# Kernel optimization log

Hardware: AMD Instinct MI355X
Metric: run time of the kernel (lower is better)

The kernel has to match this reference:

```python
import jax, jax.numpy as jnp
import numpy as np

T, H, E, K, I = 4096, 1024, 8, 2, 2048
EPS = 1e-5


def setup_inputs() -> dict:
    key = jax.random.key(0)
    ks = jax.random.split(key, 5)
    xavier = jax.nn.initializers.variance_scaling(1.0, 'fan_avg', 'uniform', dtype=jnp.float32)
    return {
        'x': jax.random.normal(ks[0], (T, H), dtype=jnp.float32),
        'scale': jnp.ones((H,), dtype=jnp.float32),
        'gate_kernel': xavier(ks[1], (H, E), jnp.float32),
        'gate_bias': jnp.zeros((E,), dtype=jnp.float32),
        'mlp1_weight': xavier(ks[2], (E, 2 * I, H), jnp.float32),
        'mlp1_bias': jnp.zeros((E, 2 * I), dtype=jnp.float32),
        'mlp2_weight': xavier(ks[3], (E, H, I), jnp.float32),
        'mlp2_bias': jnp.zeros((E, H), dtype=jnp.float32),
    }


def reference(x, scale, gate_kernel, gate_bias, mlp1_weight, mlp1_bias, mlp2_weight, mlp2_bias):
    # RMSNorm in fp32
    t = x.astype(jnp.float32)
    rms = jnp.sqrt(jnp.mean(t * t, axis=-1, keepdims=True) + EPS)
    normed = ((t / rms) * scale).astype(x.dtype)  # [T, H]

    # Gating: top-k experts + softmax over selected logits
    gate_logits = normed @ gate_kernel + gate_bias  # [T, E]
    expert_logits, expert_indices = jax.lax.top_k(gate_logits, K)  # [T, K]
    expert_weights = jax.nn.softmax(expert_logits, axis=-1)  # [T, K]

    # Dense all-expert SwiGLU MLP (faithful to vmap-over-experts original)
    # mlp1_weight: [E, 2I, H] -> mlp1: [E, T, 2I]
    mlp1 = jnp.einsum('td,efd->etf', normed, mlp1_weight) + mlp1_bias[:, None, :]
    gate_part = jnp.minimum(mlp1[..., :I], 7.0)
    linear_part = jnp.clip(mlp1[..., I:], -7.0, 7.0)
    swish_gate = gate_part * jax.nn.sigmoid(1.702 * gate_part)
    activated = swish_gate * (linear_part + 1.0)  # [E, T, I]
    # mlp2_weight: [E, H, I] -> expert_outputs: [T, E, H]
    expert_outputs = (jnp.einsum('eti,ehi->eth', activated, mlp2_weight)
                      + mlp2_bias[:, None, :]).transpose(1, 0, 2)

    # Scatter top-k weights to dense [T, E] and combine
    one_hot = jax.nn.one_hot(expert_indices, E, dtype=expert_outputs.dtype)  # [T, K, E]
    dense_gate_weights = jnp.sum(one_hot * expert_weights[..., None], axis=1)  # [T, E]
    fused = jnp.einsum('teh,te->th', expert_outputs, dense_gate_weights)
    return x + fused
```

## Files before the change

kernel.cpp:

```cpp
#include <hip/hip_runtime.h>
#include <hip/hip_bf16.h>
#include <math.h>

#define T_ 4096
#define H_ 1024
#define E_ 8
#define I_ 2048
#define EPS_ 1e-5f
#define LDST 72

using bf16x8 = __attribute__((ext_vector_type(8))) short;
using f32x4  = __attribute__((ext_vector_type(4))) float;

static __device__ __forceinline__ unsigned short f2bf(float f) {
    union { float f; unsigned int u; } v; v.f = f;
    unsigned int u = v.u;
    u += 0x7fffu + ((u >> 16) & 1u);
    return (unsigned short)(u >> 16);
}

__global__ __launch_bounds__(256) void k_convert(
    const float* __restrict__ src, unsigned short* __restrict__ dst)
{
    size_t i = (size_t)blockIdx.x * 256 + threadIdx.x;
    const float4* s = (const float4*)src + i * 2;
    float4 a = s[0], b = s[1];
    ushort4 lo, hi;
    lo.x = f2bf(a.x); lo.y = f2bf(a.y); lo.z = f2bf(a.z); lo.w = f2bf(a.w);
    hi.x = f2bf(b.x); hi.y = f2bf(b.y); hi.z = f2bf(b.z); hi.w = f2bf(b.w);
    ((ushort4*)dst)[i * 2]     = lo;
    ((ushort4*)dst)[i * 2 + 1] = hi;
}

__global__ __launch_bounds__(256) void k_norm_gate(
    const float* __restrict__ x, const float* __restrict__ scale,
    const float* __restrict__ gk, const float* __restrict__ gb,
    unsigned short* __restrict__ normed_bf,
    int* __restrict__ counts, int* __restrict__ tok_list, float* __restrict__ w_list)
{
    int t = blockIdx.x;
    int tid = threadIdx.x;
    int lane = tid & 63, wave = tid >> 6;

    float4 xv = ((const float4*)(x + (size_t)t * H_))[tid];
    float ss = xv.x*xv.x + xv.y*xv.y + xv.z*xv.z + xv.w*xv.w;
    #pragma unroll
    for (int off = 32; off; off >>= 1) ss += __shfl_down(ss, off);

    __shared__ float red[4];
    __shared__ float s_inv;
    if (lane == 0) red[wave] = ss;
    __syncthreads();
    if (tid == 0) {
        float tot = red[0] + red[1] + red[2] + red[3];
        s_inv = 1.0f / sqrtf(tot / (float)H_ + EPS_);
    }
    __syncthreads();
    float inv = s_inv;

    float4 sv = ((const float4*)scale)[tid];
    float nv[4];
    nv[0] = xv.x*inv*sv.x; nv[1] = xv.y*inv*sv.y;
    nv[2] = xv.z*inv*sv.z; nv[3] = xv.w*inv*sv.w;
    ushort4 nb;
    nb.x = f2bf(nv[0]); nb.y = f2bf(nv[1]); nb.z = f2bf(nv[2]); nb.w = f2bf(nv[3]);
    ((ushort4*)(normed_bf + (size_t)t * H_))[tid] = nb;

    float p[E_];
    #pragma unroll
    for (int e = 0; e < E_; e++) p[e] = 0.f;
    int h0 = tid * 4;
    #pragma unroll
    for (int j = 0; j < 4; j++) {
        const float4* g4 = (const float4*)(gk + (size_t)(h0 + j) * E_);
        float4 a = g4[0], b = g4[1];
        float n = nv[j];
        p[0] += n*a.x; p[1] += n*a.y; p[2] += n*a.z; p[3] += n*a.w;
        p[4] += n*b.x; p[5] += n*b.y; p[6] += n*b.z; p[7] += n*b.w;
    }
    __shared__ float pr[E_][4];
    #pragma unroll
    for (int e = 0; e < E_; e++) {
        float v = p[e];
        #pragma unroll
        for (int off = 32; off; off >>= 1) v += __shfl_down(v, off);
        if (lane == 0) pr[e][wave] = v;
    }
    __syncthreads();
    if (tid == 0) {
        float lg[E_];
        #pragma unroll
        for (int e = 0; e < E_; e++)
            lg[e] = pr[e][0] + pr[e][1] + pr[e][2] + pr[e][3] + gb[e];
        int b0 = -1, b1 = -1; float l0 = -1e30f, l1 = -1e30f;
        #pragma unroll
        for (int e = 0; e < E_; e++) {
            if (lg[e] > l0) { l1 = l0; b1 = b0; l0 = lg[e]; b0 = e; }
            else if (lg[e] > l1) { l1 = lg[e]; b1 = e; }
        }
        float e1 = expf(l1 - l0);
        float w0 = 1.f / (1.f + e1);
        float w1 = e1 / (1.f + e1);
        int p0 = atomicAdd(&counts[b0], 1);
        tok_list[b0 * T_ + p0] = t * 2 + 0; w_list[b0 * T_ + p0] = w0;
        int p1 = atomicAdd(&counts[b1], 1);
        tok_list[b1 * T_ + p1] = t * 2 + 1; w_list[b1 * T_ + p1] = w1;
    }
}

__global__ __launch_bounds__(256) void k_init_out(
    const float* __restrict__ x, float* __restrict__ out)
{
    size_t i = (size_t)blockIdx.x * 256 + threadIdx.x;
    ((float4*)out)[i] = ((const float4*)x)[i];
}

template<bool PRE>
__global__ __launch_bounds__(256) void k_mlp1(
    const float* __restrict__ w1f, const unsigned short* __restrict__ w1b,
    const float* __restrict__ b1,
    const unsigned short* __restrict__ normed_bf,
    const int* __restrict__ counts, const int* __restrict__ tok_list,
    unsigned short* __restrict__ act)
{
    int e = blockIdx.z;
    int Ne = counts[e];
    int mt0 = blockIdx.y * 64;
    if (mt0 >= Ne) return;
    int it0 = blockIdx.x * 64;
    int tid = threadIdx.x;
    int lane = tid & 63, w = tid >> 6;
    int quad = lane >> 4, m16 = lane & 15;
    int wr = w >> 1, wc = w & 1;

    __shared__ unsigned short lA[64 * LDST];
    __shared__ unsigned short lBg[64 * LDST];
    __shared__ unsigned short lBl[64 * LDST];
    __shared__ int ls_tk[64];

    if (tid < 64) {
        int slot = mt0 + tid;
        ls_tk[tid] = (slot < Ne) ? tok_list[e * T_ + slot] : -1;
    }
    __syncthreads();

    f32x4 accg[2][2], accl[2][2];
    #pragma unroll
    for (int mi = 0; mi < 2; mi++)
        #pragma unroll
        for (int ni = 0; ni < 2; ni++) {
            accg[mi][ni] = (f32x4){0.f, 0.f, 0.f, 0.f};
            accl[mi][ni] = (f32x4){0.f, 0.f, 0.f, 0.f};
        }

    const size_t w1base = (size_t)e * 2 * I_ * H_;
    int rA = tid >> 3, sgA = tid & 7;
    int nB = tid >> 2, sgB = tid & 3;

    for (int kk = 0; kk < H_; kk += 64) {
        #pragma unroll
        for (int rr = 0; rr < 64; rr += 32) {
            int r = rA + rr;
            int tk = ls_tk[r];
            uint4 v = make_uint4(0u, 0u, 0u, 0u);
            if (tk >= 0)
                v = *(const uint4*)(normed_bf + (size_t)(tk >> 1) * H_ + kk + sgA * 8);
            *(uint4*)(&lA[r * LDST + sgA * 8]) = v;
        }
        if (PRE) {
            const unsigned short* srcg = w1b + w1base + (size_t)(it0 + nB) * H_ + kk + sgB * 16;
            const unsigned short* srcl = srcg + (size_t)I_ * H_;
            *(uint4*)(&lBg[nB * LDST + sgB * 16])     = ((const uint4*)srcg)[0];
            *(uint4*)(&lBg[nB * LDST + sgB * 16 + 8]) = ((const uint4*)srcg)[1];
            *(uint4*)(&lBl[nB * LDST + sgB * 16])     = ((const uint4*)srcl)[0];
            *(uint4*)(&lBl[nB * LDST + sgB * 16 + 8]) = ((const uint4*)srcl)[1];
        } else {
            const float* srcg = w1f + w1base + (size_t)(it0 + nB) * H_ + kk + sgB * 16;
            const float* srcl = srcg + (size_t)I_ * H_;
            unsigned short tg[16], tl[16];
            #pragma unroll
            for (int q = 0; q < 4; q++) {
                float4 fg = ((const float4*)srcg)[q];
                float4 fl = ((const float4*)srcl)[q];
                tg[q*4+0] = f2bf(fg.x); tg[q*4+1] = f2bf(fg.y);
                tg[q*4+2] = f2bf(fg.z); tg[q*4+3] = f2bf(fg.w);
                tl[q*4+0] = f2bf(fl.x); tl[q*4+1] = f2bf(fl.y);
                tl[q*4+2] = f2bf(fl.z); tl[q*4+3] = f2bf(fl.w);
            }
            *(uint4*)(&lBg[nB * LDST + sgB * 16])     = *(uint4*)(&tg[0]);
            *(uint4*)(&lBg[nB * LDST + sgB * 16 + 8]) = *(uint4*)(&tg[8]);
            *(uint4*)(&lBl[nB * LDST + sgB * 16])     = *(uint4*)(&tl[0]);
            *(uint4*)(&lBl[nB * LDST + sgB * 16 + 8]) = *(uint4*)(&tl[8]);
        }
        __syncthreads();
        #pragma unroll
        for (int ks = 0; ks < 64; ks += 32) {
            bf16x8 af[2], bg[2], bl[2];
            #pragma unroll
            for (int mi = 0; mi < 2; mi++)
                af[mi] = *(const bf16x8*)(&lA[(wr * 32 + mi * 16 + m16) * LDST + ks + quad * 8]);
            #pragma unroll
            for (int ni = 0; ni < 2; ni++) {
                bg[ni] = *(const bf16x8*)(&lBg[(wc * 32 + ni * 16 + m16) * LDST + ks + quad * 8]);
                bl[ni] = *(const bf16x8*)(&lBl[(wc * 32 + ni * 16 + m16) * LDST + ks + quad * 8]);
            }
            #pragma unroll
            for (int mi = 0; mi < 2; mi++)
                #pragma unroll
                for (int ni = 0; ni < 2; ni++) {
                    accg[mi][ni] = __builtin_amdgcn_mfma_f32_16x16x32_bf16(
                        af[mi], bg[ni], accg[mi][ni], 0, 0, 0);
                    accl[mi][ni] = __builtin_amdgcn_mfma_f32_16x16x32_bf16(
                        af[mi], bl[ni], accl[mi][ni], 0, 0, 0);
                }
        }
        __syncthreads();
    }

    const float* b1g = b1 + (size_t)e * 2 * I_;
    const float* b1l = b1g + I_;
    #pragma unroll
    for (int mi = 0; mi < 2; mi++) {
        #pragma unroll
        for (int reg = 0; reg < 4; reg++) {
            int row = wr * 32 + mi * 16 + quad * 4 + reg;
            int tk = ls_tk[row];
            if (tk < 0) continue;
            #pragma unroll
            for (int ni = 0; ni < 2; ni++) {
                int i = it0 + wc * 32 + ni * 16 + m16;
                float g = accg[mi][ni][reg] + b1g[i];
                float l = accl[mi][ni][reg] + b1l[i];
                g = fminf(g, 7.f);
                l = fminf(fmaxf(l, -7.f), 7.f);
                float sw = g / (1.f + expf(-1.702f * g));
                act[(size_t)tk * I_ + i] = f2bf(sw * (l + 1.f));
            }
        }
    }
}

template<bool PRE>
__global__ __launch_bounds__(256) void k_mlp2(
    const float* __restrict__ w2f, const unsigned short* __restrict__ w2b,
    const float* __restrict__ b2,
    const unsigned short* __restrict__ act,
    const int* __restrict__ counts, const int* __restrict__ tok_list,
    const float* __restrict__ w_list,
    float* __restrict__ out)
{
    int e = blockIdx.z;
    int Ne = counts[e];
    int mt0 = blockIdx.y * 64;
    if (mt0 >= Ne) return;
    int ht0 = blockIdx.x * 128;
    int tid = threadIdx.x;
    int lane = tid & 63, w = tid >> 6;
    int quad = lane >> 4, m16 = lane & 15;
    int wr = w >> 1, wc = w & 1;

    __shared__ unsigned short lA[64 * LDST];
    __shared__ unsigned short lB[128 * LDST];
    __shared__ int ls_tk[64];
    __shared__ float ls_w[64];

    if (tid < 64) {
        int slot = mt0 + tid;
        ls_tk[tid] = (slot < Ne) ? tok_list[e * T_ + slot] : -1;
        ls_w[tid]  = (slot < Ne) ? w_list[e * T_ + slot] : 0.f;
    }
    __syncthreads();

    f32x4 acc[2][4];
    #pragma unroll
    for (int mi = 0; mi < 2; mi++)
        #pragma unroll
        for (int ni = 0; ni < 4; ni++)
            acc[mi][ni] = (f32x4){0.f, 0.f, 0.f, 0.f};

    const size_t w2base = (size_t)e * H_ * I_;
    int rA = tid >> 3, sgA = tid & 7;
    int nB = tid >> 2, sgB = tid & 3;

    for (int kk = 0; kk < I_; kk += 64) {
        #pragma unroll
        for (int rr = 0; rr < 64; rr += 32) {
            int r = rA + rr;
            int tk = ls_tk[r];
            uint4 v = make_uint4(0u, 0u, 0u, 0u);
            if (tk >= 0)
                v = *(const uint4*)(act + (size_t)tk * I_ + kk + sgA * 8);
            *(uint4*)(&lA[r * LDST + sgA * 8]) = v;
        }
        #pragma unroll
        for (int rr = 0; rr < 128; rr += 64) {
            int r = nB + rr;
            if (PRE) {
                const unsigned short* src = w2b + w2base + (size_t)(ht0 + r) * I_ + kk + sgB * 16;
                *(uint4*)(&lB[r * LDST + sgB * 16])     = ((const uint4*)src)[0];
                *(uint4*)(&lB[r * LDST + sgB * 16 + 8]) = ((const uint4*)src)[1];
            } else {
                const float* src = w2f + w2base + (size_t)(ht0 + r) * I_ + kk + sgB * 16;
                unsigned short tb[16];
                #pragma unroll
                for (int q = 0; q < 4; q++) {
                    float4 f4 = ((const float4*)src)[q];
                    tb[q*4+0] = f2bf(f4.x); tb[q*4+1] = f2bf(f4.y);
                    tb[q*4+2] = f2bf(f4.z); tb[q*4+3] = f2bf(f4.w);
                }
                *(uint4*)(&lB[r * LDST + sgB * 16])     = *(uint4*)(&tb[0]);
                *(uint4*)(&lB[r * LDST + sgB * 16 + 8]) = *(uint4*)(&tb[8]);
            }
        }
        __syncthreads();
        #pragma unroll
        for (int ks = 0; ks < 64; ks += 32) {
            bf16x8 af[2], bf[4];
            #pragma unroll
            for (int mi = 0; mi < 2; mi++)
                af[mi] = *(const bf16x8*)(&lA[(wr * 32 + mi * 16 + m16) * LDST + ks + quad * 8]);
            #pragma unroll
            for (int ni = 0; ni < 4; ni++)
                bf[ni] = *(const bf16x8*)(&lB[(wc * 64 + ni * 16 + m16) * LDST + ks + quad * 8]);
            #pragma unroll
            for (int mi = 0; mi < 2; mi++)
                #pragma unroll
                for (int ni = 0; ni < 4; ni++)
                    acc[mi][ni] = __builtin_amdgcn_mfma_f32_16x16x32_bf16(
                        af[mi], bf[ni], acc[mi][ni], 0, 0, 0);
        }
        __syncthreads();
    }

    const float* b2e = b2 + (size_t)e * H_;
    #pragma unroll
    for (int mi = 0; mi < 2; mi++) {
        #pragma unroll
        for (int reg = 0; reg < 4; reg++) {
            int row = wr * 32 + mi * 16 + quad * 4 + reg;
            int tk = ls_tk[row];
            if (tk < 0) continue;
            int t = tk >> 1;
            float wgt = ls_w[row];
            #pragma unroll
            for (int ni = 0; ni < 4; ni++) {
                int h = ht0 + wc * 64 + ni * 16 + m16;
                float v = acc[mi][ni][reg] + b2e[h];
                atomicAdd(&out[(size_t)t * H_ + h], wgt * v);
            }
        }
    }
}

extern "C" void kernel_launch(void* const* d_in, const int* in_sizes, int n_in,
                              void* d_out, int out_size, void* d_ws, size_t ws_size,
                              hipStream_t stream) {
    const float* x     = (const float*)d_in[0];
    const float* scale = (const float*)d_in[1];
    const float* gk    = (const float*)d_in[2];
    const float* gb    = (const float*)d_in[3];
    const float* w1    = (const float*)d_in[4];
    const float* b1    = (const float*)d_in[5];
    const float* w2    = (const float*)d_in[6];
    const float* b2    = (const float*)d_in[7];
    float* out = (float*)d_out;

    char* ws = (char*)d_ws;
    const size_t MB = 1024 * 1024;
    bool pre = ws_size >= (size_t)138 * MB;

    unsigned short* normed_bf = (unsigned short*)ws;
    unsigned short* act       = (unsigned short*)(ws + 8 * MB);
    unsigned short* w1b = nullptr;
    unsigned short* w2b = nullptr;
    char* ctl;
    if (pre) {
        w1b = (unsigned short*)(ws + 40 * MB);
        w2b = (unsigned short*)(ws + 104 * MB);
        ctl = ws + 136 * MB;
    } else {
        ctl = ws + 40 * MB;
    }
    int*   counts   = (int*)ctl;
    int*   tok_list = (int*)(ctl + 256);
    float* w_list   = (float*)(ctl + 256 + (size_t)E_ * T_ * 4);

    hipMemsetAsync(counts, 0, E_ * sizeof(int), stream);

    k_norm_gate<<<dim3(T_), dim3(256), 0, stream>>>(x, scale, gk, gb,
                                                    normed_bf, counts, tok_list, w_list);
    if (pre) {
        k_convert<<<dim3((E_ * 2 * I_ * H_) / (256 * 8)), dim3(256), 0, stream>>>(w1, w1b);
        k_convert<<<dim3((E_ * H_ * I_) / (256 * 8)), dim3(256), 0, stream>>>(w2, w2b);
    }
    k_init_out<<<dim3(T_ * H_ / (256 * 4)), dim3(256), 0, stream>>>(x, out);

    if (pre) {
        k_mlp1<true><<<dim3(I_ / 64, T_ / 64, E_), dim3(256), 0, stream>>>(
            nullptr, w1b, b1, normed_bf, counts, tok_list, act);
        k_mlp2<true><<<dim3(H_ / 128, T_ / 64, E_), dim3(256), 0, stream>>>(
            nullptr, w2b, b2, act, counts, tok_list, w_list, out);
    } else {
        k_mlp1<false><<<dim3(I_ / 64, T_ / 64, E_), dim3(256), 0, stream>>>(
            w1, nullptr, b1, normed_bf, counts, tok_list, act);
        k_mlp2<false><<<dim3(H_ / 128, T_ / 64, E_), dim3(256), 0, stream>>>(
            w2, nullptr, b2, act, counts, tok_list, w_list, out);
    }
}
```

Before: 603.9 us.

## Prefetch next K-tile into registers in MoE GEMMs; one token per wave in norm-gate

In the pre-converted bf16 path of both expert GEMM kernels, the next 64-wide K tile of activations and weights is loaded into registers while MFMAs run on the current LDS tile. This hides global-load latency behind compute. The norm/gate kernel now handles one token per wavefront, using xor shuffles instead of LDS reductions and block barriers. The cost is more live registers, which may lower occupancy, and the loop still uses two barriers per iteration with a single LDS buffer.

```diff
diff --git a/kernel.cpp b/kernel.cpp
--- a/kernel.cpp
+++ b/kernel.cpp
@@ -38,65 +38,65 @@
     unsigned short* __restrict__ normed_bf,
     int* __restrict__ counts, int* __restrict__ tok_list, float* __restrict__ w_list)
 {
-    int t = blockIdx.x;
     int tid = threadIdx.x;
-    int lane = tid & 63, wave = tid >> 6;
-
-    float4 xv = ((const float4*)(x + (size_t)t * H_))[tid];
-    float ss = xv.x*xv.x + xv.y*xv.y + xv.z*xv.z + xv.w*xv.w;
-    #pragma unroll
-    for (int off = 32; off; off >>= 1) ss += __shfl_down(ss, off);
-
-    __shared__ float red[4];
-    __shared__ float s_inv;
-    if (lane == 0) red[wave] = ss;
-    __syncthreads();
-    if (tid == 0) {
-        float tot = red[0] + red[1] + red[2] + red[3];
-        s_inv = 1.0f / sqrtf(tot / (float)H_ + EPS_);
-    }
-    __syncthreads();
-    float inv = s_inv;
-
-    float4 sv = ((const float4*)scale)[tid];
-    float nv[4];
-    nv[0] = xv.x*inv*sv.x; nv[1] = xv.y*inv*sv.y;
-    nv[2] = xv.z*inv*sv.z; nv[3] = xv.w*inv*sv.w;
-    ushort4 nb;
-    nb.x = f2bf(nv[0]); nb.y = f2bf(nv[1]); nb.z = f2bf(nv[2]); nb.w = f2bf(nv[3]);
-    ((ushort4*)(normed_bf + (size_t)t * H_))[tid] = nb;
+    int wave = tid >> 6, lane = tid & 63;
+    int t = blockIdx.x * 4 + wave;
+    const float* xr = x + (size_t)t * H_;
+    int h0 = lane * 16;
+
+    float4 xv[4], sv[4];
+    #pragma unroll
+    for (int c = 0; c < 4; c++) {
+        xv[c] = *(const float4*)(xr + h0 + c * 4);
+        sv[c] = *(const float4*)(scale + h0 + c * 4);
+    }
+    float ss = 0.f;
+    #pragma unroll
+    for (int c = 0; c < 4; c++)
+        ss += xv[c].x*xv[c].x + xv[c].y*xv[c].y + xv[c].z*xv[c].z + xv[c].w*xv[c].w;
+    #pragma unroll
+    for (int off = 32; off; off >>= 1) ss += __shfl_xor(ss, off);
+    float inv = 1.0f / sqrtf(ss / (float)H_ + EPS_);
+
+    float nv[16];
+    #pragma unroll
+    for (int c = 0; c < 4; c++) {
+        nv[c*4+0] = xv[c].x * inv * sv[c].x;
+        nv[c*4+1] = xv[c].y * inv * sv[c].y;
+        nv[c*4+2] = xv[c].z * inv * sv[c].z;
+        nv[c*4+3] = xv[c].w * inv * sv[c].w;
+    }
+    #pragma unroll
+    for (int c = 0; c < 4; c++) {
+        ushort4 nb;
+        nb.x = f2bf(nv[c*4+0]); nb.y = f2bf(nv[c*4+1]);
+        nb.z = f2bf(nv[c*4+2]); nb.w = f2bf(nv[c*4+3]);
+        *(ushort4*)(normed_bf + (size_t)t * H_ + h0 + c * 4) = nb;
+    }
 
     float p[E_];
     #pragma unroll
     for (int e = 0; e < E_; e++) p[e] = 0.f;
-    int h0 = tid * 4;
-    #pragma unroll
-    for (int j = 0; j < 4; j++) {
+    #pragma unroll
+    for (int j = 0; j < 16; j++) {
         const float4* g4 = (const float4*)(gk + (size_t)(h0 + j) * E_);
         float4 a = g4[0], b = g4[1];
         float n = nv[j];
         p[0] += n*a.x; p[1] += n*a.y; p[2] += n*a.z; p[3] += n*a.w;
         p[4] += n*b.x; p[5] += n*b.y; p[6] += n*b.z; p[7] += n*b.w;
     }
-    __shared__ float pr[E_][4];
     #pragma unroll
     for (int e = 0; e < E_; e++) {
-        float v = p[e];
-        #pragma unroll
-        for (int off = 32; off; off >>= 1) v += __shfl_down(v, off);
-        if (lane == 0) pr[e][wave] = v;
-    }
-    __syncthreads();
-    if (tid == 0) {
-        float lg[E_];
-        #pragma unroll
-        for (int e = 0; e < E_; e++)
-            lg[e] = pr[e][0] + pr[e][1] + pr[e][2] + pr[e][3] + gb[e];
+        #pragma unroll
+        for (int off = 32; off; off >>= 1) p[e] += __shfl_xor(p[e], off);
+    }
+    if (lane == 0) {
         int b0 = -1, b1 = -1; float l0 = -1e30f, l1 = -1e30f;
         #pragma unroll
         for (int e = 0; e < E_; e++) {
-            if (lg[e] > l0) { l1 = l0; b1 = b0; l0 = lg[e]; b0 = e; }
-            else if (lg[e] > l1) { l1 = lg[e]; b1 = e; }
+            float lg = p[e] + gb[e];
+            if (lg > l0) { l1 = l0; b1 = b0; l0 = lg; b0 = e; }
+            else if (lg > l1) { l1 = lg; b1 = e; }
         }
         float e1 = expf(l1 - l0);
         float w0 = 1.f / (1.f + e1);
@@ -157,64 +157,110 @@
     int rA = tid >> 3, sgA = tid & 7;
     int nB = tid >> 2, sgB = tid & 3;
 
-    for (int kk = 0; kk < H_; kk += 64) {
-        #pragma unroll
-        for (int rr = 0; rr < 64; rr += 32) {
-            int r = rA + rr;
-            int tk = ls_tk[r];
-            uint4 v = make_uint4(0u, 0u, 0u, 0u);
-            if (tk >= 0)
-                v = *(const uint4*)(normed_bf + (size_t)(tk >> 1) * H_ + kk + sgA * 8);
-            *(uint4*)(&lA[r * LDST + sgA * 8]) = v;
-        }
-        if (PRE) {
-            const unsigned short* srcg = w1b + w1base + (size_t)(it0 + nB) * H_ + kk + sgB * 16;
-            const unsigned short* srcl = srcg + (size_t)I_ * H_;
-            *(uint4*)(&lBg[nB * LDST + sgB * 16])     = ((const uint4*)srcg)[0];
-            *(uint4*)(&lBg[nB * LDST + sgB * 16 + 8]) = ((const uint4*)srcg)[1];
-            *(uint4*)(&lBl[nB * LDST + sgB * 16])     = ((const uint4*)srcl)[0];
-            *(uint4*)(&lBl[nB * LDST + sgB * 16 + 8]) = ((const uint4*)srcl)[1];
-        } else {
-            const float* srcg = w1f + w1base + (size_t)(it0 + nB) * H_ + kk + sgB * 16;
-            const float* srcl = srcg + (size_t)I_ * H_;
-            unsigned short tg[16], tl[16];
-            #pragma unroll
-            for (int q = 0; q < 4; q++) {
-                float4 fg = ((const float4*)srcg)[q];
-                float4 fl = ((const float4*)srcl)[q];
-                tg[q*4+0] = f2bf(fg.x); tg[q*4+1] = f2bf(fg.y);
-                tg[q*4+2] = f2bf(fg.z); tg[q*4+3] = f2bf(fg.w);
-                tl[q*4+0] = f2bf(fl.x); tl[q*4+1] = f2bf(fl.y);
-                tl[q*4+2] = f2bf(fl.z); tl[q*4+3] = f2bf(fl.w);
-            }
-            *(uint4*)(&lBg[nB * LDST + sgB * 16])     = *(uint4*)(&tg[0]);
-            *(uint4*)(&lBg[nB * LDST + sgB * 16 + 8]) = *(uint4*)(&tg[8]);
-            *(uint4*)(&lBl[nB * LDST + sgB * 16])     = *(uint4*)(&tl[0]);
-            *(uint4*)(&lBl[nB * LDST + sgB * 16 + 8]) = *(uint4*)(&tl[8]);
-        }
-        __syncthreads();
-        #pragma unroll
-        for (int ks = 0; ks < 64; ks += 32) {
-            bf16x8 af[2], bg[2], bl[2];
-            #pragma unroll
-            for (int mi = 0; mi < 2; mi++)
-                af[mi] = *(const bf16x8*)(&lA[(wr * 32 + mi * 16 + m16) * LDST + ks + quad * 8]);
-            #pragma unroll
-            for (int ni = 0; ni < 2; ni++) {
-                bg[ni] = *(const bf16x8*)(&lBg[(wc * 32 + ni * 16 + m16) * LDST + ks + quad * 8]);
-                bl[ni] = *(const bf16x8*)(&lBl[(wc * 32 + ni * 16 + m16) * LDST + ks + quad * 8]);
-            }
-            #pragma unroll
-            for (int mi = 0; mi < 2; mi++)
+    if (PRE) {
+        int tk0 = ls_tk[rA], tk1 = ls_tk[rA + 32];
+        const unsigned short* sA0 = normed_bf + (size_t)((tk0 < 0) ? 0 : (tk0 >> 1)) * H_ + sgA * 8;
+        const unsigned short* sA1 = normed_bf + (size_t)((tk1 < 0) ? 0 : (tk1 >> 1)) * H_ + sgA * 8;
+        const unsigned short* sG = w1b + w1base + (size_t)(it0 + nB) * H_ + sgB * 16;
+        const unsigned short* sL = sG + (size_t)I_ * H_;
+
+        uint4 ra0, ra1, rg0, rg1, rl0, rl1;
+        ra0 = (tk0 >= 0) ? *(const uint4*)(sA0) : make_uint4(0,0,0,0);
+        ra1 = (tk1 >= 0) ? *(const uint4*)(sA1) : make_uint4(0,0,0,0);
+        rg0 = ((const uint4*)sG)[0]; rg1 = ((const uint4*)sG)[1];
+        rl0 = ((const uint4*)sL)[0]; rl1 = ((const uint4*)sL)[1];
+
+        for (int kk = 0; kk < H_; kk += 64) {
+            __syncthreads();
+            *(uint4*)(&lA[rA * LDST + sgA * 8])          = ra0;
+            *(uint4*)(&lA[(rA + 32) * LDST + sgA * 8])   = ra1;
+            *(uint4*)(&lBg[nB * LDST + sgB * 16])        = rg0;
+            *(uint4*)(&lBg[nB * LDST + sgB * 16 + 8])    = rg1;
+            *(uint4*)(&lBl[nB * LDST + sgB * 16])        = rl0;
+            *(uint4*)(&lBl[nB * LDST + sgB * 16 + 8])    = rl1;
+            __syncthreads();
+            if (kk + 64 < H_) {
+                int k2 = kk + 64;
+                ra0 = (tk0 >= 0) ? *(const uint4*)(sA0 + k2) : make_uint4(0,0,0,0);
+                ra1 = (tk1 >= 0) ? *(const uint4*)(sA1 + k2) : make_uint4(0,0,0,0);
+                rg0 = ((const uint4*)(sG + k2))[0]; rg1 = ((const uint4*)(sG + k2))[1];
+                rl0 = ((const uint4*)(sL + k2))[0]; rl1 = ((const uint4*)(sL + k2))[1];
+            }
+            #pragma unroll
+            for (int ks = 0; ks < 64; ks += 32) {
+                bf16x8 af[2], bg[2], bl[2];
+                #pragma unroll
+                for (int mi = 0; mi < 2; mi++)
+                    af[mi] = *(const bf16x8*)(&lA[(wr * 32 + mi * 16 + m16) * LDST + ks + quad * 8]);
                 #pragma unroll
                 for (int ni = 0; ni < 2; ni++) {
-                    accg[mi][ni] = __builtin_amdgcn_mfma_f32_16x16x32_bf16(
-                        af[mi], bg[ni], accg[mi][ni], 0, 0, 0);
-                    accl[mi][ni] = __builtin_amdgcn_mfma_f32_16x16x32_bf16(
-                        af[mi], bl[ni], accl[mi][ni], 0, 0, 0);
+                    bg[ni] = *(const bf16x8*)(&lBg[(wc * 32 + ni * 16 + m16) * LDST + ks + quad * 8]);
+                    bl[ni] = *(const bf16x8*)(&lBl[(wc * 32 + ni * 16 + m16) * LDST + ks + quad * 8]);
                 }
-        }
-        __syncthreads();
+                #pragma unroll
+                for (int mi = 0; mi < 2; mi++)
+                    #pragma unroll
+                    for (int ni = 0; ni < 2; ni++) {
+                        accg[mi][ni] = __builtin_amdgcn_mfma_f32_16x16x32_bf16(
+                            af[mi], bg[ni], accg[mi][ni], 0, 0, 0);
+                        accl[mi][ni] = __builtin_amdgcn_mfma_f32_16x16x32_bf16(
+                            af[mi], bl[ni], accl[mi][ni], 0, 0, 0);
+                    }
+            }
+        }
+    } else {
+        for (int kk = 0; kk < H_; kk += 64) {
+            #pragma unroll
+            for (int rr = 0; rr < 64; rr += 32) {
+                int r = rA + rr;
+                int tk = ls_tk[r];
+                uint4 v = make_uint4(0u, 0u, 0u, 0u);
+                if (tk >= 0)
+                    v = *(const uint4*)(normed_bf + (size_t)(tk >> 1) * H_ + kk + sgA * 8);
+                *(uint4*)(&lA[r * LDST + sgA * 8]) = v;
+            }
+            {
+                const float* srcg = w1f + w1base + (size_t)(it0 + nB) * H_ + kk + sgB * 16;
+                const float* srcl = srcg + (size_t)I_ * H_;
+                unsigned short tg[16], tl[16];
+                #pragma unroll
+                for (int q = 0; q < 4; q++) {
+                    float4 fg = ((const float4*)srcg)[q];
+                    float4 fl = ((const float4*)srcl)[q];
+                    tg[q*4+0] = f2bf(fg.x); tg[q*4+1] = f2bf(fg.y);
+                    tg[q*4+2] = f2bf(fg.z); tg[q*4+3] = f2bf(fg.w);
+                    tl[q*4+0] = f2bf(fl.x); tl[q*4+1] = f2bf(fl.y);
+                    tl[q*4+2] = f2bf(fl.z); tl[q*4+3] = f2bf(fl.w);
+                }
+                *(uint4*)(&lBg[nB * LDST + sgB * 16])     = *(uint4*)(&tg[0]);
+                *(uint4*)(&lBg[nB * LDST + sgB * 16 + 8]) = *(uint4*)(&tg[8]);
+                *(uint4*)(&lBl[nB * LDST + sgB * 16])     = *(uint4*)(&tl[0]);
+                *(uint4*)(&lBl[nB * LDST + sgB * 16 + 8]) = *(uint4*)(&tl[8]);
+            }
+            __syncthreads();
+            #pragma unroll
+            for (int ks = 0; ks < 64; ks += 32) {
+                bf16x8 af[2], bg[2], bl[2];
+                #pragma unroll
+                for (int mi = 0; mi < 2; mi++)
+                    af[mi] = *(const bf16x8*)(&lA[(wr * 32 + mi * 16 + m16) * LDST + ks + quad * 8]);
+                #pragma unroll
+                for (int ni = 0; ni < 2; ni++) {
+                    bg[ni] = *(const bf16x8*)(&lBg[(wc * 32 + ni * 16 + m16) * LDST + ks + quad * 8]);
+                    bl[ni] = *(const bf16x8*)(&lBl[(wc * 32 + ni * 16 + m16) * LDST + ks + quad * 8]);
+                }
+                #pragma unroll
+                for (int mi = 0; mi < 2; mi++)
+                    #pragma unroll
+                    for (int ni = 0; ni < 2; ni++) {
+                        accg[mi][ni] = __builtin_amdgcn_mfma_f32_16x16x32_bf16(
+                            af[mi], bg[ni], accg[mi][ni], 0, 0, 0);
+                        accl[mi][ni] = __builtin_amdgcn_mfma_f32_16x16x32_bf16(
+                            af[mi], bl[ni], accl[mi][ni], 0, 0, 0);
+                    }
+            }
+            __syncthreads();
+        }
     }
 
     const float* b1g = b1 + (size_t)e * 2 * I_;
@@ -282,24 +328,66 @@
     int rA = tid >> 3, sgA = tid & 7;
     int nB = tid >> 2, sgB = tid & 3;
 
-    for (int kk = 0; kk < I_; kk += 64) {
-        #pragma unroll
-        for (int rr = 0; rr < 64; rr += 32) {
-            int r = rA + rr;
-            int tk = ls_tk[r];
-            uint4 v = make_uint4(0u, 0u, 0u, 0u);
-            if (tk >= 0)
-                v = *(const uint4*)(act + (size_t)tk * I_ + kk + sgA * 8);
-            *(uint4*)(&lA[r * LDST + sgA * 8]) = v;
-        }
-        #pragma unroll
-        for (int rr = 0; rr < 128; rr += 64) {
-            int r = nB + rr;
-            if (PRE) {
-                const unsigned short* src = w2b + w2base + (size_t)(ht0 + r) * I_ + kk + sgB * 16;
-                *(uint4*)(&lB[r * LDST + sgB * 16])     = ((const uint4*)src)[0];
-                *(uint4*)(&lB[r * LDST + sgB * 16 + 8]) = ((const uint4*)src)[1];
-            } else {
+    if (PRE) {
+        int tk0 = ls_tk[rA], tk1 = ls_tk[rA + 32];
+        const unsigned short* sA0 = act + (size_t)((tk0 < 0) ? 0 : tk0) * I_ + sgA * 8;
+        const unsigned short* sA1 = act + (size_t)((tk1 < 0) ? 0 : tk1) * I_ + sgA * 8;
+        const unsigned short* sB0 = w2b + w2base + (size_t)(ht0 + nB) * I_ + sgB * 16;
+        const unsigned short* sB1 = sB0 + (size_t)64 * I_;
+
+        uint4 ra0, ra1, rb00, rb01, rb10, rb11;
+        ra0 = (tk0 >= 0) ? *(const uint4*)(sA0) : make_uint4(0,0,0,0);
+        ra1 = (tk1 >= 0) ? *(const uint4*)(sA1) : make_uint4(0,0,0,0);
+        rb00 = ((const uint4*)sB0)[0]; rb01 = ((const uint4*)sB0)[1];
+        rb10 = ((const uint4*)sB1)[0]; rb11 = ((const uint4*)sB1)[1];
+
+        for (int kk = 0; kk < I_; kk += 64) {
+            __syncthreads();
+            *(uint4*)(&lA[rA * LDST + sgA * 8])            = ra0;
+            *(uint4*)(&lA[(rA + 32) * LDST + sgA * 8])     = ra1;
+            *(uint4*)(&lB[nB * LDST + sgB * 16])           = rb00;
+            *(uint4*)(&lB[nB * LDST + sgB * 16 + 8])       = rb01;
+            *(uint4*)(&lB[(nB + 64) * LDST + sgB * 16])    = rb10;
+            *(uint4*)(&lB[(nB + 64) * LDST + sgB * 16 + 8])= rb11;
+            __syncthreads();
+            if (kk + 64 < I_) {
+                int k2 = kk + 64;
+                ra0 = (tk0 >= 0) ? *(const uint4*)(sA0 + k2) : make_uint4(0,0,0,0);
+                ra1 = (tk1 >= 0) ? *(const uint4*)(sA1 + k2) : make_uint4(0,0,0,0);
+                rb00 = ((const uint4*)(sB0 + k2))[0]; rb01 = ((const uint4*)(sB0 + k2))[1];
+                rb10 = ((const uint4*)(sB1 + k2))[0]; rb11 = ((const uint4*)(sB1 + k2))[1];
+            }
+            #pragma unroll
+            for (int ks = 0; ks < 64; ks += 32) {
+                bf16x8 af[2], bf[4];
+                #pragma unroll
+                for (int mi = 0; mi < 2; mi++)
+                    af[mi] = *(const bf16x8*)(&lA[(wr * 32 + mi * 16 + m16) * LDST + ks + quad * 8]);
+                #pragma unroll
+                for (int ni = 0; ni < 4; ni++)
+                    bf[ni] = *(const bf16x8*)(&lB[(wc * 64 + ni * 16 + m16) * LDST + ks + quad * 8]);
+                #pragma unroll
+                for (int mi = 0; mi < 2; mi++)
+                    #pragma unroll
+                    for (int ni = 0; ni < 4; ni++)
+                        acc[mi][ni] = __builtin_amdgcn_mfma_f32_16x16x32_bf16(
+                            af[mi], bf[ni], acc[mi][ni], 0, 0, 0);
+            }
+        }
+    } else {
+        for (int kk = 0; kk < I_; kk += 64) {
+            #pragma unroll
+            for (int rr = 0; rr < 64; rr += 32) {
+                int r = rA + rr;
+                int tk = ls_tk[r];
+                uint4 v = make_uint4(0u, 0u, 0u, 0u);
+                if (tk >= 0)
+                    v = *(const uint4*)(act + (size_t)tk * I_ + kk + sgA * 8);
+                *(uint4*)(&lA[r * LDST + sgA * 8]) = v;
+            }
+            #pragma unroll
+            for (int rr = 0; rr < 128; rr += 64) {
+                int r = nB + rr;
                 const float* src = w2f + w2base + (size_t)(ht0 + r) * I_ + kk + sgB * 16;
                 unsigned short tb[16];
                 #pragma unroll
@@ -311,25 +399,25 @@
                 *(uint4*)(&lB[r * LDST + sgB * 16])     = *(uint4*)(&tb[0]);
                 *(uint4*)(&lB[r * LDST + sgB * 16 + 8]) = *(uint4*)(&tb[8]);
             }
-        }
-        __syncthreads();
-        #pragma unroll
-        for (int ks = 0; ks < 64; ks += 32) {
-            bf16x8 af[2], bf[4];
-            #pragma unroll
-            for (int mi = 0; mi < 2; mi++)
-                af[mi] = *(const bf16x8*)(&lA[(wr * 32 + mi * 16 + m16) * LDST + ks + quad * 8]);
-            #pragma unroll
-            for (int ni = 0; ni < 4; ni++)
-                bf[ni] = *(const bf16x8*)(&lB[(wc * 64 + ni * 16 + m16) * LDST + ks + quad * 8]);
-            #pragma unroll
-            for (int mi = 0; mi < 2; mi++)
+            __syncthreads();
+            #pragma unroll
+            for (int ks = 0; ks < 64; ks += 32) {
+                bf16x8 af[2], bf[4];
+                #pragma unroll
+                for (int mi = 0; mi < 2; mi++)
+                    af[mi] = *(const bf16x8*)(&lA[(wr * 32 + mi * 16 + m16) * LDST + ks + quad * 8]);
                 #pragma unroll
                 for (int ni = 0; ni < 4; ni++)
-                    acc[mi][ni] = __builtin_amdgcn_mfma_f32_16x16x32_bf16(
-                        af[mi], bf[ni], acc[mi][ni], 0, 0, 0);
-        }
-        __syncthreads();
+                    bf[ni] = *(const bf16x8*)(&lB[(wc * 64 + ni * 16 + m16) * LDST + ks + quad * 8]);
+                #pragma unroll
+                for (int mi = 0; mi < 2; mi++)
+                    #pragma unroll
+                    for (int ni = 0; ni < 4; ni++)
+                        acc[mi][ni] = __builtin_amdgcn_mfma_f32_16x16x32_bf16(
+                            af[mi], bf[ni], acc[mi][ni], 0, 0, 0);
+            }
+            __syncthreads();
+        }
     }
 
     const float* b2e = b2 + (size_t)e * H_;
@@ -387,8 +475,8 @@
 
     hipMemsetAsync(counts, 0, E_ * sizeof(int), stream);
 
-    k_norm_gate<<<dim3(T_), dim3(256), 0, stream>>>(x, scale, gk, gb,
-                                                    normed_bf, counts, tok_list, w_list);
+    k_norm_gate<<<dim3(T_ / 4), dim3(256), 0, stream>>>(x, scale, gk, gb,
+                                                        normed_bf, counts, tok_list, w_list);
     if (pre) {
         k_convert<<<dim3((E_ * 2 * I_ * H_) / (256 * 8)), dim3(256), 0, stream>>>(w1, w1b);
         k_convert<<<dim3((E_ * H_ * I_) / (256 * 8)), dim3(256), 0, stream>>>(w2, w2b);
```

Result: no change. 599.8 us (-0.7%).
